# Optimization experiments

Hardware: AMD Instinct MI355X
Metric: run time of the kernel (lower is better)

Reference implementation:

```python
import jax, jax.numpy as jnp
import numpy as np

N_NODES = 100000
N_EDGES = 1000000
F_IN = 256
HID = 256
HID2 = 128
N_CLS = 2


def setup_inputs() -> dict:
    key = jax.random.key(0)
    ks = jax.random.split(key, 8)
    x = jax.random.normal(ks[0], (N_NODES, F_IN), dtype=jnp.float32)
    edge_index = jax.random.randint(ks[1], (2, N_EDGES), 0, N_NODES, dtype=jnp.int64)
    s = lambda k, shp: jax.random.normal(k, shp, dtype=jnp.float32) / np.sqrt(shp[0])
    return {
        "x": x,
        "edge_index": edge_index,
        "W1l": s(ks[2], (F_IN, HID)),
        "W1r": s(ks[3], (F_IN, HID)),
        "b1": jnp.zeros((HID,), jnp.float32),
        "W2l": s(ks[4], (HID, HID2)),
        "W2r": s(ks[5], (HID, HID2)),
        "b2": jnp.zeros((HID2,), jnp.float32),
        "Wc": s(ks[6], (HID2, N_CLS)),
        "bc": jnp.zeros((N_CLS,), jnp.float32),
    }


def _sage_conv(x, src, dst, deg_inv, Wl, Wr, b):
    # mean-aggregate neighbor (source) features at each destination node
    msg = x[src]                                              # [E, F]
    agg = jax.ops.segment_sum(msg, dst, num_segments=N_NODES)  # [N, F]
    mean = agg * deg_inv[:, None]                             # zero for isolated nodes
    return mean @ Wl + b + x @ Wr


def reference(x, edge_index, W1l, W1r, b1, W2l, W2r, b2, Wc, bc):
    src, dst = edge_index[0], edge_index[1]
    cnt = jax.ops.segment_sum(jnp.ones((N_EDGES,), x.dtype), dst, num_segments=N_NODES)
    deg_inv = jnp.where(cnt > 0, 1.0 / jnp.maximum(cnt, 1.0), 0.0)
    h = jax.nn.relu(_sage_conv(x, src, dst, deg_inv, W1l, W1r, b1))   # dropout is identity in eval
    h = jax.nn.relu(_sage_conv(h, src, dst, deg_inv, W2l, W2r, b2))
    logits = h @ Wc + bc
    return jax.nn.log_softmax(logits, axis=1)
```

## Files before the change

### kernel.cpp

```cpp
#include <hip/hip_runtime.h>
#include <hip/hip_bf16.h>

#define NN 100000
#define NE 1000000
#define MPAD 100096

typedef __attribute__((ext_vector_type(8))) short bf16x8;
typedef __attribute__((ext_vector_type(4))) float f32x4;
typedef __attribute__((ext_vector_type(8))) unsigned short us8;

static __device__ __forceinline__ float bf2f(unsigned short u){
  unsigned int x = ((unsigned int)u) << 16;
  return __uint_as_float(x);
}
static __device__ __forceinline__ unsigned short f2bf(float f){
  unsigned int x = __float_as_uint(f);
  unsigned int r = (x + 0x7fffu + ((x >> 16) & 1u)) >> 16;
  return (unsigned short)r;
}
static __device__ __forceinline__ void gld16(const void* g, void* l){
  __builtin_amdgcn_global_load_lds((const __attribute__((address_space(1))) void*)g,
                                   (__attribute__((address_space(3))) void*)l, 16, 0, 0);
}


__global__ void k_degree(const int* __restrict__ dst, int* __restrict__ cnt, int E){
  int e = blockIdx.x * blockDim.x + threadIdx.x;
  if (e < E) atomicAdd(&cnt[dst[e]], 1);
}

__global__ void k_chunk_sum(const int* __restrict__ cnt, int* __restrict__ partials, int N){
  __shared__ int sw[16];
  int b = blockIdx.x, t = threadIdx.x;
  int i = b * 1024 + t;
  int v = (i < N) ? cnt[i] : 0;
  #pragma unroll
  for (int off = 32; off; off >>= 1) v += __shfl_xor(v, off);
  int lane = t & 63, w = t >> 6;
  if (lane == 0) sw[w] = v;
  __syncthreads();
  if (t < 16){
    int s = sw[t];
    #pragma unroll
    for (int off = 8; off; off >>= 1) s += __shfl_xor(s, off);
    if (t == 0) partials[b] = s;
  }
}

__global__ void k_scan_partials(const int* __restrict__ partials, int* __restrict__ bases, int nchunk){
  if (threadIdx.x == 0 && blockIdx.x == 0){
    int run = 0;
    for (int j = 0; j < nchunk; j++){ bases[j] = run; run += partials[j]; }
  }
}

__global__ void k_chunk_scan(const int* __restrict__ cnt, const int* __restrict__ bases,
                             int* __restrict__ offs, int* __restrict__ cursor,
                             float* __restrict__ deginv, int N){
  __shared__ int sd[1024];
  int b = blockIdx.x, t = threadIdx.x;
  int i = b * 1024 + t;
  int v = (i < N) ? cnt[i] : 0;
  sd[t] = v;
  __syncthreads();
  for (int off = 1; off < 1024; off <<= 1){
    int x = (t >= off) ? sd[t - off] : 0;
    __syncthreads();
    sd[t] += x;
    __syncthreads();
  }
  if (i < N){
    int excl = bases[b] + sd[t] - v;
    offs[i] = excl;
    cursor[i] = excl;
    deginv[i] = (v > 0) ? (1.0f / (float)v) : 0.0f;
  }
}

__global__ void k_fill(const int* __restrict__ src, const int* __restrict__ dst,
                       int* __restrict__ cursor, int* __restrict__ csr, int E){
  int e = blockIdx.x * blockDim.x + threadIdx.x;
  if (e < E){
    int p = atomicAdd(&cursor[dst[e]], 1);
    csr[p] = src[e];
  }
}


__global__ void k_cvt(const float* __restrict__ x, unsigned short* __restrict__ xb){
  size_t i = ((size_t)blockIdx.x * 256 + threadIdx.x) * 8;
  if (i >= (size_t)MPAD * 256) return;
  int row = (int)(i >> 8);
  us8 o;
  if (row < NN){
    const float4* p = (const float4*)(x + i);
    float4 a = p[0], b = p[1];
    o[0]=f2bf(a.x); o[1]=f2bf(a.y); o[2]=f2bf(a.z); o[3]=f2bf(a.w);
    o[4]=f2bf(b.x); o[5]=f2bf(b.y); o[6]=f2bf(b.z); o[7]=f2bf(b.w);
  } else {
    #pragma unroll
    for (int j = 0; j < 8; j++) o[j] = 0;
  }
  *(us8*)(xb + i) = o;
}


__global__ void k_prep_w(const float* __restrict__ W1l, const float* __restrict__ W1r,
                         const float* __restrict__ W2l, const float* __restrict__ W2r,
                         unsigned short* __restrict__ Bt1, unsigned short* __restrict__ Bt2){
  int i = blockIdx.x * 256 + threadIdx.x;
  if (i < 512 * 256){
    int n = i >> 8, k = i & 255;
    float v = (n < 256) ? W1l[k * 256 + n] : W1r[k * 256 + (n - 256)];
    Bt1[n * 256 + k] = f2bf(v);
  }
  if (i < 256 * 256){
    int n = i >> 8, k = i & 255;
    float v = (n < 128) ? W2l[k * 128 + n] : W2r[k * 128 + (n - 128)];
    Bt2[n * 256 + k] = f2bf(v);
  }
}


__global__ __launch_bounds__(256)
void k_gemm(const unsigned short* __restrict__ A,
            const unsigned short* __restrict__ Bt,
            unsigned short* __restrict__ C,
            int Nout)
{
  __shared__ __align__(16) unsigned short lA[128 * 64];
  __shared__ __align__(16) unsigned short lB[128 * 64];
  const int t = threadIdx.x;
  const int lane = t & 63, wid = t >> 6;
  const int wm = wid >> 1, wn = wid & 1;
  const int m0 = blockIdx.x * 128;
  const int n0 = blockIdx.y * 128;

  f32x4 acc[4][4] = {};

  const int strow = wid * 32 + (lane >> 3);
  const int sc    = (lane & 7) ^ ((lane >> 3) & 7);

  for (int kt = 0; kt < 4; ++kt){
    __syncthreads();
    #pragma unroll
    for (int s4 = 0; s4 < 4; ++s4){
      int row = strow + s4 * 8;
      gld16(A  + (size_t)(m0 + row) * 256 + kt * 64 + sc * 8, &lA[(wid * 4 + s4) * 512]);
      gld16(Bt + (size_t)(n0 + row) * 256 + kt * 64 + sc * 8, &lB[(wid * 4 + s4) * 512]);
    }
    __syncthreads();
    #pragma unroll
    for (int ks = 0; ks < 2; ++ks){
      bf16x8 av[4], bv[4];
      const int kc = ks * 4 + (lane >> 4);
      #pragma unroll
      for (int m = 0; m < 4; m++){
        int r = wm * 64 + m * 16 + (lane & 15);
        av[m] = *(const bf16x8*)&lA[r * 64 + ((kc ^ (r & 7)) << 3)];
      }
      #pragma unroll
      for (int n = 0; n < 4; n++){
        int c = wn * 64 + n * 16 + (lane & 15);
        bv[n] = *(const bf16x8*)&lB[c * 64 + ((kc ^ (c & 7)) << 3)];
      }
      #pragma unroll
      for (int m = 0; m < 4; m++)
        #pragma unroll
        for (int n = 0; n < 4; n++)
          acc[m][n] = __builtin_amdgcn_mfma_f32_16x16x32_bf16(av[m], bv[n], acc[m][n], 0, 0, 0);
    }
  }

  const int crow0 = m0 + wm * 64 + (lane >> 4) * 4;
  const int ccol0 = n0 + wn * 64 + (lane & 15);
  #pragma unroll
  for (int m = 0; m < 4; m++){
    #pragma unroll
    for (int r = 0; r < 4; r++){
      size_t rowoff = (size_t)(crow0 + m * 16 + r) * Nout;
      #pragma unroll
      for (int n = 0; n < 4; n++)
        C[rowoff + ccol0 + n * 16] = f2bf(acc[m][n][r]);
    }
  }
}


__global__ void k_agg1(const unsigned short* __restrict__ C1,
                       const float* __restrict__ b1,
                       const int* __restrict__ offs, const int* __restrict__ cnt,
                       const float* __restrict__ deginv,
                       const int* __restrict__ csr,
                       unsigned short* __restrict__ h, int N)
{
  int wv = threadIdx.x >> 6, lane = threadIdx.x & 63;
  int n = blockIdx.x * 4 + wv;
  if (n >= N) return;
  int beg = offs[n], d = cnt[n];
  const int g = lane >> 5;
  const int cl = lane & 31;

  float acc[8];
  #pragma unroll
  for (int k = 0; k < 8; k++) acc[k] = 0.f;

  for (int w0 = 0; w0 < d; w0 += 64){
    int wlen = min(d - w0, 64);
    int idx = 0;
    if (lane < wlen) idx = csr[beg + w0 + lane];
    int nIter = (wlen + 7) >> 3;
    for (int t = 0; t < nIter; t++){
      int e0 = t * 8 + g;
      int s0 = __shfl(idx, e0);
      int s1 = __shfl(idx, e0 + 2);
      int s2 = __shfl(idx, e0 + 4);
      int s3 = __shfl(idx, e0 + 6);
      us8 v0 = *(const us8*)(C1 + (size_t)s0 * 512 + cl * 8);
      us8 v1 = *(const us8*)(C1 + (size_t)s1 * 512 + cl * 8);
      us8 v2 = *(const us8*)(C1 + (size_t)s2 * 512 + cl * 8);
      us8 v3 = *(const us8*)(C1 + (size_t)s3 * 512 + cl * 8);
      if (e0 < wlen){
        #pragma unroll
        for (int k = 0; k < 8; k++) acc[k] += bf2f(v0[k]);
      }
      if (e0 + 2 < wlen){
        #pragma unroll
        for (int k = 0; k < 8; k++) acc[k] += bf2f(v1[k]);
      }
      if (e0 + 4 < wlen){
        #pragma unroll
        for (int k = 0; k < 8; k++) acc[k] += bf2f(v2[k]);
      }
      if (e0 + 6 < wlen){
        #pragma unroll
        for (int k = 0; k < 8; k++) acc[k] += bf2f(v3[k]);
      }
    }
  }
  #pragma unroll
  for (int k = 0; k < 8; k++) acc[k] += __shfl_xor(acc[k], 32);

  if (lane < 32){
    float di = deginv[n];
    us8 rv = *(const us8*)(C1 + (size_t)n * 512 + 256 + cl * 8);
    float4 b0 = *(const float4*)(b1 + cl * 8);
    float4 b4 = *(const float4*)(b1 + cl * 8 + 4);
    float bb[8] = {b0.x, b0.y, b0.z, b0.w, b4.x, b4.y, b4.z, b4.w};
    us8 o;
    #pragma unroll
    for (int k = 0; k < 8; k++)
      o[k] = f2bf(fmaxf(acc[k] * di + bf2f(rv[k]) + bb[k], 0.f));
    *(us8*)(h + (size_t)n * 256 + cl * 8) = o;
  }
}


__global__ void k_agg2cls(const unsigned short* __restrict__ C2,
                          const float* __restrict__ b2,
                          const float* __restrict__ Wc,
                          const float* __restrict__ bc,
                          const int* __restrict__ offs, const int* __restrict__ cnt,
                          const float* __restrict__ deginv,
                          const int* __restrict__ csr,
                          float* __restrict__ out, int N)
{
  int wv = threadIdx.x >> 6, lane = threadIdx.x & 63;
  int n = blockIdx.x * 4 + wv;
  if (n >= N) return;
  int beg = offs[n], d = cnt[n];
  const int g = lane >> 4;
  const int cl = lane & 15;

  float acc[8];
  #pragma unroll
  for (int k = 0; k < 8; k++) acc[k] = 0.f;

  for (int w0 = 0; w0 < d; w0 += 64){
    int wlen = min(d - w0, 64);
    int idx = 0;
    if (lane < wlen) idx = csr[beg + w0 + lane];
    int nIter = (wlen + 15) >> 4;
    for (int t = 0; t < nIter; t++){
      int e0 = t * 16 + g;
      int s0 = __shfl(idx, e0);
      int s1 = __shfl(idx, e0 + 4);
      int s2 = __shfl(idx, e0 + 8);
      int s3 = __shfl(idx, e0 + 12);
      us8 v0 = *(const us8*)(C2 + (size_t)s0 * 256 + cl * 8);
      us8 v1 = *(const us8*)(C2 + (size_t)s1 * 256 + cl * 8);
      us8 v2 = *(const us8*)(C2 + (size_t)s2 * 256 + cl * 8);
      us8 v3 = *(const us8*)(C2 + (size_t)s3 * 256 + cl * 8);
      if (e0 < wlen){
        #pragma unroll
        for (int k = 0; k < 8; k++) acc[k] += bf2f(v0[k]);
      }
      if (e0 + 4 < wlen){
        #pragma unroll
        for (int k = 0; k < 8; k++) acc[k] += bf2f(v1[k]);
      }
      if (e0 + 8 < wlen){
        #pragma unroll
        for (int k = 0; k < 8; k++) acc[k] += bf2f(v2[k]);
      }
      if (e0 + 12 < wlen){
        #pragma unroll
        for (int k = 0; k < 8; k++) acc[k] += bf2f(v3[k]);
      }
    }
  }
  #pragma unroll
  for (int k = 0; k < 8; k++){
    acc[k] += __shfl_xor(acc[k], 16);
    acc[k] += __shfl_xor(acc[k], 32);
  }

  float di = deginv[n];
  us8 rv = *(const us8*)(C2 + (size_t)n * 256 + 128 + cl * 8);
  float4 b0 = *(const float4*)(b2 + cl * 8);
  float4 b4 = *(const float4*)(b2 + cl * 8 + 4);
  float bb[8] = {b0.x, b0.y, b0.z, b0.w, b4.x, b4.y, b4.z, b4.w};
  float p0 = 0.f, p1 = 0.f;
  #pragma unroll
  for (int k = 0; k < 8; k += 2){
    float h0 = fmaxf(acc[k]     * di + bf2f(rv[k])     + bb[k],     0.f);
    float h1 = fmaxf(acc[k + 1] * di + bf2f(rv[k + 1]) + bb[k + 1], 0.f);
    float4 w = *(const float4*)(Wc + (cl * 8 + k) * 2);
    p0 += h0 * w.x + h1 * w.z;
    p1 += h0 * w.y + h1 * w.w;
  }
  #pragma unroll
  for (int off = 8; off; off >>= 1){
    p0 += __shfl_xor(p0, off);
    p1 += __shfl_xor(p1, off);
  }
  if (lane == 0){
    float z0 = p0 + bc[0], z1 = p1 + bc[1];
    float m = fmaxf(z0, z1);
    float lse = m + logf(expf(z0 - m) + expf(z1 - m));
    out[(size_t)n * 2 + 0] = z0 - lse;
    out[(size_t)n * 2 + 1] = z1 - lse;
  }
}


extern "C" void kernel_launch(void* const* d_in, const int* in_sizes, int n_in,
                              void* d_out, int out_size, void* d_ws, size_t ws_size,
                              hipStream_t stream)
{
  const float* x   = (const float*)d_in[0];
  const int*   ei  = (const int*)d_in[1];
  const float* W1l = (const float*)d_in[2];
  const float* W1r = (const float*)d_in[3];
  const float* b1  = (const float*)d_in[4];
  const float* W2l = (const float*)d_in[5];
  const float* W2r = (const float*)d_in[6];
  const float* b2  = (const float*)d_in[7];
  const float* Wc  = (const float*)d_in[8];
  const float* bc  = (const float*)d_in[9];
  float* out = (float*)d_out;

  const int N = NN, E = NE;
  const int* src = ei;
  const int* dst = ei + E;

  char* ws = (char*)d_ws;
  size_t off = 0;
  auto alloc = [&](size_t bytes) -> void* {
    void* p = ws + off;
    off += (bytes + 255) & ~(size_t)255;
    return p;
  };
  int*   cnt      = (int*)alloc((size_t)N * 4);
  int*   offs     = (int*)alloc((size_t)N * 4);
  int*   cursor   = (int*)alloc((size_t)N * 4);
  float* deginv   = (float*)alloc((size_t)N * 4);
  int*   partials = (int*)alloc(1024);
  int*   bases    = (int*)alloc(1024);
  int*   csr      = (int*)alloc((size_t)E * 4);
  unsigned short* Bt1 = (unsigned short*)alloc((size_t)512 * 256 * 2);
  unsigned short* Bt2 = (unsigned short*)alloc((size_t)256 * 256 * 2);
  unsigned short* xb  = (unsigned short*)alloc((size_t)MPAD * 256 * 2);
  unsigned short* C1  = (unsigned short*)alloc((size_t)MPAD * 512 * 2);

  unsigned short* h  = xb;
  unsigned short* C2 = C1;

  (void)in_sizes; (void)n_in; (void)out_size; (void)ws_size;

  hipMemsetAsync(cnt, 0, (size_t)N * 4, stream);

  int nchunk = (N + 1023) / 1024;
  k_degree<<<(E + 255) / 256, 256, 0, stream>>>(dst, cnt, E);
  k_chunk_sum<<<nchunk, 1024, 0, stream>>>(cnt, partials, N);
  k_scan_partials<<<1, 64, 0, stream>>>(partials, bases, nchunk);
  k_chunk_scan<<<nchunk, 1024, 0, stream>>>(cnt, bases, offs, cursor, deginv, N);
  k_fill<<<(E + 255) / 256, 256, 0, stream>>>(src, dst, cursor, csr, E);

  k_cvt<<<MPAD / 8, 256, 0, stream>>>(x, xb);
  k_prep_w<<<512, 256, 0, stream>>>(W1l, W1r, W2l, W2r, Bt1, Bt2);

  {
    dim3 g(MPAD / 128, 512 / 128);
    k_gemm<<<g, 256, 0, stream>>>(xb, Bt1, C1, 512);
  }
  k_agg1<<<N / 4, 256, 0, stream>>>(C1, b1, offs, cnt, deginv, csr, h, N);

  {
    dim3 g(MPAD / 128, 256 / 128);
    k_gemm<<<g, 256, 0, stream>>>(h, Bt2, C2, 256);
  }
  k_agg2cls<<<N / 4, 256, 0, stream>>>(C2, b2, Wc, bc, offs, cnt, deginv, csr, out, N);
}
```

Baseline: 368.4 us.

## Store layer-1 neighbor projections as FP8 in column-sliced layout for gather

The first GEMM now writes the neighbor-projection half (Wl columns) as software-encoded FP8 (e4m3-style) into 8 column slices of 32 bytes per node. The root half stays bf16 in a separate buffer. The layer-1 aggregation kernel is split into 8 slices per node group, each gathering 4-byte words from the compact slice layout, so each gather stays within a node's 32-byte slice. The partials scan is also folded into the chunk-scan kernel, removing a serial single-thread launch. This trades precision (FP8 mantissa) and 8x more blocks for less gather traffic, which risks accuracy tolerance.

```diff
diff --git a/kernel.cpp b/kernel.cpp
--- a/kernel.cpp
+++ b/kernel.cpp
@@ -17,6 +17,22 @@
   unsigned int x = __float_as_uint(f);
   unsigned int r = (x + 0x7fffu + ((x >> 16) & 1u)) >> 16;
   return (unsigned short)r;
+}
+static __device__ __forceinline__ unsigned char f2fp8(float f){
+  unsigned int u = __float_as_uint(f);
+  unsigned int s = (u >> 24) & 0x80u;
+  unsigned int au = u & 0x7FFFFFFFu;
+  if (au >= 0x43E00000u) return (unsigned char)(s | 0x7Eu);
+  if (au <  0x3C800000u) return (unsigned char)s;
+  unsigned int r = au + 0x7FFFFu + ((au >> 20) & 1u);
+  return (unsigned char)(s | ((r >> 20) - 960u));
+}
+static __device__ __forceinline__ void dec4f(unsigned int v, float& r0, float& r1, float& r2, float& r3){
+  unsigned int b0 = v & 0xFFu, b1 = (v >> 8) & 0xFFu, b2 = (v >> 16) & 0xFFu, b3 = (v >> 24);
+  r0 = __uint_as_float((((b0 & 0x7Fu) + 960u) << 20) | ((b0 & 0x80u) << 24));
+  r1 = __uint_as_float((((b1 & 0x7Fu) + 960u) << 20) | ((b1 & 0x80u) << 24));
+  r2 = __uint_as_float((((b2 & 0x7Fu) + 960u) << 20) | ((b2 & 0x80u) << 24));
+  r3 = __uint_as_float((((b3 & 0x7Fu) + 960u) << 20) | ((b3 & 0x80u) << 24));
 }
 static __device__ __forceinline__ void gld16(const void* g, void* l){
   __builtin_amdgcn_global_load_lds((const __attribute__((address_space(1))) void*)g,
@@ -47,22 +63,23 @@
   }
 }
 
-__global__ void k_scan_partials(const int* __restrict__ partials, int* __restrict__ bases, int nchunk){
-  if (threadIdx.x == 0 && blockIdx.x == 0){
-    int run = 0;
-    for (int j = 0; j < nchunk; j++){ bases[j] = run; run += partials[j]; }
-  }
-}
-
-__global__ void k_chunk_scan(const int* __restrict__ cnt, const int* __restrict__ bases,
+__global__ void k_chunk_scan(const int* __restrict__ cnt, const int* __restrict__ partials,
+                             int nchunk,
                              int* __restrict__ offs, int* __restrict__ cursor,
                              float* __restrict__ deginv, int N){
   __shared__ int sd[1024];
+  __shared__ int sp[128];
   int b = blockIdx.x, t = threadIdx.x;
+  if (t < 128) sp[t] = (t < b && t < nchunk) ? partials[t] : 0;
   int i = b * 1024 + t;
   int v = (i < N) ? cnt[i] : 0;
   sd[t] = v;
   __syncthreads();
+  #pragma unroll
+  for (int off = 64; off; off >>= 1){
+    if (t < off) sp[t] += sp[t + off];
+    __syncthreads();
+  }
   for (int off = 1; off < 1024; off <<= 1){
     int x = (t >= off) ? sd[t - off] : 0;
     __syncthreads();
@@ -70,7 +87,7 @@
     __syncthreads();
   }
   if (i < N){
-    int excl = bases[b] + sd[t] - v;
+    int excl = sp[0] + sd[t] - v;
     offs[i] = excl;
     cursor[i] = excl;
     deginv[i] = (v > 0) ? (1.0f / (float)v) : 0.0f;
@@ -122,10 +139,12 @@
 }
 
 
+template<bool SPLIT>
 __global__ __launch_bounds__(256)
 void k_gemm(const unsigned short* __restrict__ A,
             const unsigned short* __restrict__ Bt,
             unsigned short* __restrict__ C,
+            unsigned char* __restrict__ Q8,
             int Nout)
 {
   __shared__ __align__(16) unsigned short lA[128 * 64];
@@ -174,84 +193,106 @@
 
   const int crow0 = m0 + wm * 64 + (lane >> 4) * 4;
   const int ccol0 = n0 + wn * 64 + (lane & 15);
-  #pragma unroll
-  for (int m = 0; m < 4; m++){
-    #pragma unroll
-    for (int r = 0; r < 4; r++){
-      size_t rowoff = (size_t)(crow0 + m * 16 + r) * Nout;
+  if (SPLIT && n0 < 256){
+    #pragma unroll
+    for (int m = 0; m < 4; m++){
       #pragma unroll
-      for (int n = 0; n < 4; n++)
-        C[rowoff + ccol0 + n * 16] = f2bf(acc[m][n][r]);
-    }
-  }
-}
-
-
-__global__ void k_agg1(const unsigned short* __restrict__ C1,
+      for (int r = 0; r < 4; r++){
+        int row = crow0 + m * 16 + r;
+        #pragma unroll
+        for (int n = 0; n < 4; n++){
+          int col = ccol0 + n * 16;
+          Q8[((size_t)(col >> 5) * MPAD + row) * 32 + (col & 31)] = f2fp8(acc[m][n][r]);
+        }
+      }
+    }
+  } else {
+    const int stride = SPLIT ? 256 : Nout;
+    const int cbase  = SPLIT ? (ccol0 - 256) : ccol0;
+    #pragma unroll
+    for (int m = 0; m < 4; m++){
+      #pragma unroll
+      for (int r = 0; r < 4; r++){
+        size_t rowoff = (size_t)(crow0 + m * 16 + r) * stride;
+        #pragma unroll
+        for (int n = 0; n < 4; n++)
+          C[rowoff + cbase + n * 16] = f2bf(acc[m][n][r]);
+      }
+    }
+  }
+}
+
+
+__global__ void k_agg1(const unsigned char* __restrict__ Q8,
+                       const unsigned short* __restrict__ R1,
                        const float* __restrict__ b1,
                        const int* __restrict__ offs, const int* __restrict__ cnt,
                        const float* __restrict__ deginv,
                        const int* __restrict__ csr,
                        unsigned short* __restrict__ h, int N)
 {
-  int wv = threadIdx.x >> 6, lane = threadIdx.x & 63;
-  int n = blockIdx.x * 4 + wv;
+  const int bid = blockIdx.x;
+  const int slice = bid & 7;
+  const int chunk = bid >> 3;
+  const int wv = threadIdx.x >> 6, lane = threadIdx.x & 63;
+  const int n = chunk * 4 + wv;
   if (n >= N) return;
-  int beg = offs[n], d = cnt[n];
-  const int g = lane >> 5;
-  const int cl = lane & 31;
-
-  float acc[8];
-  #pragma unroll
-  for (int k = 0; k < 8; k++) acc[k] = 0.f;
+  const int beg = offs[n], d = cnt[n];
+  const int g = lane >> 3;
+  const int c = lane & 7;
+  const unsigned char* Qs = Q8 + (size_t)slice * MPAD * 32 + c * 4;
+
+  float a0 = 0.f, a1 = 0.f, a2 = 0.f, a3 = 0.f;
 
   for (int w0 = 0; w0 < d; w0 += 64){
     int wlen = min(d - w0, 64);
     int idx = 0;
     if (lane < wlen) idx = csr[beg + w0 + lane];
-    int nIter = (wlen + 7) >> 3;
+    int nIter = (wlen + 31) >> 5;
     for (int t = 0; t < nIter; t++){
-      int e0 = t * 8 + g;
+      int e0 = t * 32 + g;
       int s0 = __shfl(idx, e0);
-      int s1 = __shfl(idx, e0 + 2);
-      int s2 = __shfl(idx, e0 + 4);
-      int s3 = __shfl(idx, e0 + 6);
-      us8 v0 = *(const us8*)(C1 + (size_t)s0 * 512 + cl * 8);
-      us8 v1 = *(const us8*)(C1 + (size_t)s1 * 512 + cl * 8);
-      us8 v2 = *(const us8*)(C1 + (size_t)s2 * 512 + cl * 8);
-      us8 v3 = *(const us8*)(C1 + (size_t)s3 * 512 + cl * 8);
+      int s1 = __shfl(idx, e0 + 8);
+      int s2 = __shfl(idx, e0 + 16);
+      int s3 = __shfl(idx, e0 + 24);
+      unsigned int v0 = *(const unsigned int*)(Qs + (size_t)s0 * 32);
+      unsigned int v1 = *(const unsigned int*)(Qs + (size_t)s1 * 32);
+      unsigned int v2 = *(const unsigned int*)(Qs + (size_t)s2 * 32);
+      unsigned int v3 = *(const unsigned int*)(Qs + (size_t)s3 * 32);
+      float d0, d1, d2, d3;
       if (e0 < wlen){
-        #pragma unroll
-        for (int k = 0; k < 8; k++) acc[k] += bf2f(v0[k]);
-      }
-      if (e0 + 2 < wlen){
-        #pragma unroll
-        for (int k = 0; k < 8; k++) acc[k] += bf2f(v1[k]);
-      }
-      if (e0 + 4 < wlen){
-        #pragma unroll
-        for (int k = 0; k < 8; k++) acc[k] += bf2f(v2[k]);
-      }
-      if (e0 + 6 < wlen){
-        #pragma unroll
-        for (int k = 0; k < 8; k++) acc[k] += bf2f(v3[k]);
-      }
-    }
-  }
-  #pragma unroll
-  for (int k = 0; k < 8; k++) acc[k] += __shfl_xor(acc[k], 32);
-
-  if (lane < 32){
+        dec4f(v0, d0, d1, d2, d3); a0 += d0; a1 += d1; a2 += d2; a3 += d3;
+      }
+      if (e0 + 8 < wlen){
+        dec4f(v1, d0, d1, d2, d3); a0 += d0; a1 += d1; a2 += d2; a3 += d3;
+      }
+      if (e0 + 16 < wlen){
+        dec4f(v2, d0, d1, d2, d3); a0 += d0; a1 += d1; a2 += d2; a3 += d3;
+      }
+      if (e0 + 24 < wlen){
+        dec4f(v3, d0, d1, d2, d3); a0 += d0; a1 += d1; a2 += d2; a3 += d3;
+      }
+    }
+  }
+  #pragma unroll
+  for (int off = 8; off < 64; off <<= 1){
+    a0 += __shfl_xor(a0, off);
+    a1 += __shfl_xor(a1, off);
+    a2 += __shfl_xor(a2, off);
+    a3 += __shfl_xor(a3, off);
+  }
+
+  if (lane < 8){
+    const int col0 = slice * 32 + c * 4;
     float di = deginv[n];
-    us8 rv = *(const us8*)(C1 + (size_t)n * 512 + 256 + cl * 8);
-    float4 b0 = *(const float4*)(b1 + cl * 8);
-    float4 b4 = *(const float4*)(b1 + cl * 8 + 4);
-    float bb[8] = {b0.x, b0.y, b0.z, b0.w, b4.x, b4.y, b4.z, b4.w};
-    us8 o;
-    #pragma unroll
-    for (int k = 0; k < 8; k++)
-      o[k] = f2bf(fmaxf(acc[k] * di + bf2f(rv[k]) + bb[k], 0.f));
-    *(us8*)(h + (size_t)n * 256 + cl * 8) = o;
+    ushort4 rv = *(const ushort4*)(R1 + (size_t)n * 256 + col0);
+    float4  bv = *(const float4*)(b1 + col0);
+    ushort4 o;
+    o.x = f2bf(fmaxf(a0 * di + bf2f(rv.x) + bv.x, 0.f));
+    o.y = f2bf(fmaxf(a1 * di + bf2f(rv.y) + bv.y, 0.f));
+    o.z = f2bf(fmaxf(a2 * di + bf2f(rv.z) + bv.z, 0.f));
+    o.w = f2bf(fmaxf(a3 * di + bf2f(rv.w) + bv.w, 0.f));
+    *(ushort4*)(h + (size_t)n * 256 + col0) = o;
   }
 }
 
@@ -376,15 +417,15 @@
   int*   cursor   = (int*)alloc((size_t)N * 4);
   float* deginv   = (float*)alloc((size_t)N * 4);
   int*   partials = (int*)alloc(1024);
-  int*   bases    = (int*)alloc(1024);
   int*   csr      = (int*)alloc((size_t)E * 4);
   unsigned short* Bt1 = (unsigned short*)alloc((size_t)512 * 256 * 2);
   unsigned short* Bt2 = (unsigned short*)alloc((size_t)256 * 256 * 2);
   unsigned short* xb  = (unsigned short*)alloc((size_t)MPAD * 256 * 2);
-  unsigned short* C1  = (unsigned short*)alloc((size_t)MPAD * 512 * 2);
+  unsigned char*  Q8  = (unsigned char*)alloc((size_t)8 * MPAD * 32);
+  unsigned short* R1  = (unsigned short*)alloc((size_t)MPAD * 256 * 2);
 
   unsigned short* h  = xb;
-  unsigned short* C2 = C1;
+  unsigned short* C2 = R1;
 
   (void)in_sizes; (void)n_in; (void)out_size; (void)ws_size;
 
@@ -393,8 +434,7 @@
   int nchunk = (N + 1023) / 1024;
   k_degree<<<(E + 255) / 256, 256, 0, stream>>>(dst, cnt, E);
   k_chunk_sum<<<nchunk, 1024, 0, stream>>>(cnt, partials, N);
-  k_scan_partials<<<1, 64, 0, stream>>>(partials, bases, nchunk);
-  k_chunk_scan<<<nchunk, 1024, 0, stream>>>(cnt, bases, offs, cursor, deginv, N);
+  k_chunk_scan<<<nchunk, 1024, 0, stream>>>(cnt, partials, nchunk, offs, cursor, deginv, N);
   k_fill<<<(E + 255) / 256, 256, 0, stream>>>(src, dst, cursor, csr, E);
 
   k_cvt<<<MPAD / 8, 256, 0, stream>>>(x, xb);
@@ -402,13 +442,13 @@
 
   {
     dim3 g(MPAD / 128, 512 / 128);
-    k_gemm<<<g, 256, 0, stream>>>(xb, Bt1, C1, 512);
-  }
-  k_agg1<<<N / 4, 256, 0, stream>>>(C1, b1, offs, cnt, deginv, csr, h, N);
+    k_gemm<true><<<g, 256, 0, stream>>>(xb, Bt1, R1, Q8, 512);
+  }
+  k_agg1<<<(N / 4) * 8, 256, 0, stream>>>(Q8, R1, b1, offs, cnt, deginv, csr, h, N);
 
   {
     dim3 g(MPAD / 128, 256 / 128);
-    k_gemm<<<g, 256, 0, stream>>>(h, Bt2, C2, 256);
+    k_gemm<false><<<g, 256, 0, stream>>>(h, Bt2, C2, (unsigned char*)nullptr, 256);
   }
   k_agg2cls<<<N / 4, 256, 0, stream>>>(C2, b2, Wc, bc, offs, cnt, deginv, csr, out, N);
 }
```

Result: slower. 535.8 us (+45.4%).
